# Performance work log

Hardware: AMD Instinct MI355X
Metric: run time of the kernel (lower is better)

Reference implementation:

```python
import jax, jax.numpy as jnp
import numpy as np

R = 2        # pixel-shuffle upscale
CN = 32      # channel_nums
COL = 3      # colors
NM = 6       # module_nums (2 convs each -> 12 backbone convs)
QMAX_A = 255.0   # uint8 activation fake-quant range
QMAX_W = 127.0   # int8 (narrow) weight fake-quant range


def fq_act(x, s):
    # Brevitas Uint8ActPerTensorFloat fake-quant with STE
    v = x / s
    q = jnp.clip(jnp.round(v), 0.0, QMAX_A)
    return s * (v + jax.lax.stop_gradient(q - v))


def fq_w(w, s):
    # Int8WeightPerTensorFloat (symmetric, narrow range) fake-quant with STE
    v = w / s
    q = jnp.clip(jnp.round(v), -QMAX_W, QMAX_W)
    return s * (v + jax.lax.stop_gradient(q - v))


def conv3(x, w, b):
    y = jax.lax.conv_general_dilated(
        x, w, window_strides=(1, 1), padding=((1, 1), (1, 1)),
        dimension_numbers=("NCHW", "OIHW", "NCHW"))
    return y + b[None, :, None, None]


def qblock(x, w, b, sw, act_s):
    # QuantConv3X3: quant_in -> quant conv (+bias) -> QuantReLU (relu + quant)
    xq = fq_act(x, act_s)
    y = conv3(xq, fq_w(w, sw), b)
    y = jax.nn.relu(y)
    return fq_act(y, act_s)


def pixel_shuffle(x, r):
    B, C, H, W = x.shape
    c = C // (r * r)
    x = x.reshape(B, c, r, r, H, W)
    x = x.transpose(0, 1, 4, 2, 5, 3)   # B, c, H, r, W, r
    return x.reshape(B, c, H * r, W * r)


def _forward(x, head_w, head_b, head_sw, bb_w, bb_b, bb_sw, tr_w, tr_b, tr_sw, act_s):
    y0 = qblock(x, head_w, head_b, head_sw, act_s)

    def step(y, p):
        w, b, sw = p
        return qblock(y, w, b, sw, act_s), None

    y, _ = jax.lax.scan(step, y0, (bb_w, bb_b, bb_sw))
    y = qblock(y + y0, tr_w, tr_b, tr_sw, act_s)   # act_type='linear' still hits QuantReLU branch
    y = jnp.clip(y, 0.0, 255.0)
    return pixel_shuffle(y, R)


def setup_inputs() -> dict:
    key = jax.random.key(0)
    ks = jax.random.split(key, 4)
    B, H, W = 8, 256, 256
    x = jax.random.uniform(ks[0], (B, COL, H, W), dtype=jnp.float32) * 255.0
    head_w = jax.random.normal(ks[1], (CN, COL, 3, 3), dtype=jnp.float32) * 0.05
    head_b = jnp.zeros((CN,), jnp.float32)
    bb_w = jax.random.normal(ks[2], (2 * NM, CN, CN, 3, 3), dtype=jnp.float32) * 0.05
    bb_b = jnp.zeros((2 * NM, CN), jnp.float32)
    tr_w = jax.random.normal(ks[3], (COL * R * R, CN, 3, 3), dtype=jnp.float32) * 0.05
    tr_b = jnp.zeros((COL * R * R,), jnp.float32)
    head_sw = jnp.max(jnp.abs(head_w)) / QMAX_W
    bb_sw = jnp.max(jnp.abs(bb_w), axis=(1, 2, 3, 4)) / QMAX_W
    tr_sw = jnp.max(jnp.abs(tr_w)) / QMAX_W
    act_s = jnp.float32(1.0)
    return dict(x=x, head_w=head_w, head_b=head_b, head_sw=head_sw,
                bb_w=bb_w, bb_b=bb_b, bb_sw=bb_sw,
                tr_w=tr_w, tr_b=tr_b, tr_sw=tr_sw, act_s=act_s)


def reference(x, head_w, head_b, head_sw, bb_w, bb_b, bb_sw, tr_w, tr_b, tr_sw, act_s):
    return _forward(x, head_w, head_b, head_sw, bb_w, bb_b, bb_sw, tr_w, tr_b, tr_sw, act_s)
```

## Files before the change

### kernel.cpp

```cpp
#include <hip/hip_runtime.h>

typedef int i32x4  __attribute__((ext_vector_type(4)));
typedef int i32x16 __attribute__((ext_vector_type(16)));

__global__ __launch_bounds__(256) void quantw_kernel(
    const float* __restrict__ src, float* __restrict__ dst,
    const float* __restrict__ sw, int per_layer_sw, int OC, int ICK, int total)
{
    int i = blockIdx.x * 256 + threadIdx.x;
    if (i >= total) return;
    int per = OC * ICK;
    int l = i / per;
    int rem = i - l * per;
    int oc = rem / ICK;
    int k = rem - oc * ICK;
    float s = sw[per_layer_sw ? l : 0];
    float v = rintf(src[i] / s);
    v = fminf(fmaxf(v, -127.0f), 127.0f);
    dst[l * per + k * OC + oc] = v;
}

__global__ __launch_bounds__(256) void packw_i8_kernel(
    const float* __restrict__ src, signed char* __restrict__ dst,
    const float* __restrict__ sw, int per_layer_sw, int OC_real, int total)
{
    int i = blockIdx.x * 256 + threadIdx.x;
    if (i >= total) return;
    int l   = i / 9216;
    int r   = i - l * 9216;
    int tap = r >> 10;
    int r2  = r & 1023;
    int lane = r2 >> 4;
    int j   = r2 & 15;
    int oc  = lane & 31;
    int ic  = ((lane >> 5) << 4) + j;
    signed char v = 0;
    if (oc < OC_real) {
        float s = sw[per_layer_sw ? l : 0];
        float q = rintf(src[((l * OC_real + oc) * 32 + ic) * 9 + tap] / s);
        q = fminf(fmaxf(q, -127.0f), 127.0f);
        v = (signed char)(int)q;
    }
    dst[i] = v;
}

__global__ __launch_bounds__(256) void wsum_kernel(
    const float* __restrict__ bb_w, const float* __restrict__ bb_sw,
    const float* __restrict__ tr_w, const float* __restrict__ tr_sw,
    float* __restrict__ wsum)
{
    int t = blockIdx.x * 256 + threadIdx.x;
    if (t >= 416) return;
    int l = t >> 5, oc = t & 31;
    float sum = 0.0f;
    if (l < 12) {
        float s = bb_sw[l];
        for (int k = 0; k < 288; ++k) {
            float q = rintf(bb_w[(l * 32 + oc) * 288 + k] / s);
            sum += fminf(fmaxf(q, -127.0f), 127.0f);
        }
    } else if (oc < 12) {
        float s = tr_sw[0];
        for (int k = 0; k < 288; ++k) {
            float q = rintf(tr_w[oc * 288 + k] / s);
            sum += fminf(fmaxf(q, -127.0f), 127.0f);
        }
    }
    wsum[t] = sum;
}

__global__ __launch_bounds__(256) void head_kernel(
    const float* __restrict__ x, const float* __restrict__ wq,
    const float* __restrict__ bias, const float* __restrict__ sw_ptr,
    const float* __restrict__ s_ptr, unsigned char* __restrict__ out)
{
    __shared__ unsigned char tile[3][10][34];
    const int tid = threadIdx.x;
    const int x0 = blockIdx.x * 32;
    const int y0 = blockIdx.y * 8;
    const int b  = blockIdx.z;
    const float s = s_ptr[0];

    for (int ch = 0; ch < 3; ++ch) {
        const int base = (b * 3 + ch) << 16;
        for (int p = tid; p < 10 * 34; p += 256) {
            int r = p / 34, c = p - r * 34;
            int gy = y0 + r - 1, gx = x0 + c - 1;
            unsigned char v = 0;
            if ((unsigned)gy < 256u && (unsigned)gx < 256u) {
                float xv = x[base + (gy << 8) + gx];
                float q = (s == 1.0f) ? xv : (xv / s);
                q = rintf(q);
                q = fminf(fmaxf(q, 0.0f), 255.0f);
                v = (unsigned char)q;
            }
            tile[ch][r][c] = v;
        }
    }
    __syncthreads();

    const int c = tid & 31, r = tid >> 5;
    float acc[32];
    #pragma unroll
    for (int i = 0; i < 32; ++i) acc[i] = 0.0f;

    #pragma unroll
    for (int ic = 0; ic < 3; ++ic) {
        float a[9];
        #pragma unroll
        for (int dy = 0; dy < 3; ++dy)
            #pragma unroll
            for (int dx = 0; dx < 3; ++dx)
                a[dy * 3 + dx] = (float)tile[ic][r + dy][c + dx];
        #pragma unroll
        for (int t = 0; t < 9; ++t) {
            const float* wrow = wq + (ic * 9 + t) * 32;
            #pragma unroll
            for (int oc = 0; oc < 32; ++oc)
                acc[oc] = fmaf(a[t], wrow[oc], acc[oc]);
        }
    }

    const float alpha = s * sw_ptr[0];
    unsigned int w8[8] = {0,0,0,0,0,0,0,0};
    #pragma unroll
    for (int oc = 0; oc < 32; ++oc) {
        float y = fmaf(alpha, acc[oc], bias[oc]);
        y = fmaxf(y, 0.0f);
        float v = (s == 1.0f) ? y : (y / s);
        v = rintf(v);
        v = fminf(fmaxf(v, 0.0f), 255.0f);
        w8[oc >> 2] |= ((unsigned int)(unsigned char)v) << (8 * (oc & 3));
    }
    uint4* dst = (uint4*)(out + (size_t)((((b << 8) + (y0 + r)) << 8) + (x0 + c)) * 32);
    dst[0] = make_uint4(w8[0] ^ 0x80808080u, w8[1] ^ 0x80808080u, w8[2] ^ 0x80808080u, w8[3] ^ 0x80808080u);
    dst[1] = make_uint4(w8[4] ^ 0x80808080u, w8[5] ^ 0x80808080u, w8[6] ^ 0x80808080u, w8[7] ^ 0x80808080u);
}

template<bool FINAL>
__global__ __launch_bounds__(256, 4) void qconv_i8_kernel(
    const unsigned char* __restrict__ in,
    const unsigned char* __restrict__ resid,
    const signed char* __restrict__ Wp,
    const float* __restrict__ bias,
    const float* __restrict__ wsum,
    const float* __restrict__ sw_ptr, int sw_idx,
    const float* __restrict__ s_ptr,
    void* __restrict__ out)
{
    __shared__ unsigned char aT[19584];
    const int tid = threadIdx.x;
    const int x0 = blockIdx.x << 5;
    const int y0 = blockIdx.y << 4;
    const int b  = blockIdx.z;

    #pragma unroll
    for (int it = 0; it < 5; ++it) {
        int ci = tid + it * 256;
        if (ci < 1224) {
            int row = (ci * 241) >> 14;
            int rem = ci - row * 68;
            int xt = rem >> 1, hf = rem & 1;
            int gy = y0 + row - 1, gx = x0 + xt - 1;
            uint4 v = make_uint4(0x80808080u, 0x80808080u, 0x80808080u, 0x80808080u);
            if ((unsigned)gy < 256u && (unsigned)gx < 256u) {
                size_t off = (size_t)((((b << 8) + gy) << 8) + gx) * 32 + (hf << 4);
                v = *(const uint4*)(in + off);
                if (FINAL) {
                    uint4 rv = *(const uint4*)(resid + off);
                    unsigned int* vp = (unsigned int*)&v;
                    const unsigned int* rp = (const unsigned int*)&rv;
                    #pragma unroll
                    for (int w = 0; w < 4; ++w) {
                        unsigned int xw = vp[w], yw = rp[w], ow = 0;
                        #pragma unroll
                        for (int bb = 0; bb < 4; ++bb) {
                            int xs = (int)(signed char)(xw >> (8 * bb));
                            int ys = (int)(signed char)(yw >> (8 * bb));
                            int t = xs + ys + 128;
                            if (t > 127) t = 127;
                            ow |= ((unsigned int)(t & 255)) << (8 * bb);
                        }
                        vp[w] = ow;
                    }
                }
            }
            int cs = rem ^ ((rem >> 3) & 7);
            *(uint4*)&aT[(row * 68 + cs) << 4] = v;
        }
    }
    __syncthreads();

    const int lane = tid & 63;
    const int wid  = tid >> 6;
    const int px   = lane & 31;
    const int khf  = lane >> 5;
    const int py0  = wid << 2;
    const int gx   = x0 + px;

    i32x16 acc[4];
    #pragma unroll
    for (int p = 0; p < 4; ++p)
        #pragma unroll
        for (int i = 0; i < 16; ++i) acc[p][i] = 0;

    #pragma unroll
    for (int dx = 0; dx < 3; ++dx) {
        const int c  = ((px + dx) << 1) + khf;
        const int cs = c ^ ((c >> 3) & 7);
        i32x4 af[6];
        #pragma unroll
        for (int yl = 0; yl < 6; ++yl)
            af[yl] = *(const i32x4*)&aT[((py0 + yl) * 68 + cs) << 4];
        #pragma unroll
        for (int dy = 0; dy < 3; ++dy) {
            i32x4 wf = *(const i32x4*)(Wp + ((((dy * 3 + dx) << 6) + lane) << 4));
            acc[0] = __builtin_amdgcn_mfma_i32_32x32x32_i8(wf, af[dy + 0], acc[0], 0, 0, 0);
            acc[1] = __builtin_amdgcn_mfma_i32_32x32x32_i8(wf, af[dy + 1], acc[1], 0, 0, 0);
            acc[2] = __builtin_amdgcn_mfma_i32_32x32x32_i8(wf, af[dy + 2], acc[2], 0, 0, 0);
            acc[3] = __builtin_amdgcn_mfma_i32_32x32x32_i8(wf, af[dy + 3], acc[3], 0, 0, 0);
        }
    }

    const float s = s_ptr[0];
    const float alpha = s * sw_ptr[sw_idx];

    if (!FINAL) {
        float bv[16];
        #pragma unroll
        for (int r = 0; r < 16; ++r) {
            const int oc = (r & 3) + ((r >> 2) << 3) + (khf << 2);
            bv[r] = fmaf(alpha * 128.0f, wsum[oc], bias[oc]);
        }
        #pragma unroll
        for (int py = 0; py < 4; ++py) {
            const int gy = y0 + py0 + py;
            unsigned char* pout = (unsigned char*)out + (((size_t)((((b << 8) + gy) << 8) + gx)) << 5);
            #pragma unroll
            for (int q = 0; q < 4; ++q) {
                unsigned int wv = 0;
                #pragma unroll
                for (int j = 0; j < 4; ++j) {
                    float y = fmaf(alpha, (float)acc[py][4 * q + j], bv[4 * q + j]);
                    y = fmaxf(y, 0.0f);
                    float v = (s == 1.0f) ? y : (y / s);
                    v = rintf(v);
                    v = fminf(fmaxf(v, 0.0f), 255.0f);
                    wv |= ((unsigned int)v) << (8 * j);
                }
                *(unsigned int*)(pout + 8 * q + 4 * khf) = wv ^ 0x80808080u;
            }
        }
    } else {
        #pragma unroll
        for (int py = 0; py < 4; ++py) {
            const int gy = y0 + py0 + py;
            #pragma unroll
            for (int r = 0; r < 16; ++r) {
                const int oc = (r & 3) + ((r >> 2) << 3) + (khf << 2);
                if (oc < 12) {
                    float y = fmaf(alpha, (float)acc[py][r],
                                   fmaf(alpha * 128.0f, wsum[oc], bias[oc]));
                    y = fmaxf(y, 0.0f);
                    float v = (s == 1.0f) ? y : (y / s);
                    v = rintf(v);
                    v = fminf(fmaxf(v, 0.0f), 255.0f);
                    float o = (s == 1.0f) ? v : fminf(fmaxf(s * v, 0.0f), 255.0f);
                    const int cc = oc >> 2, r1 = (oc >> 1) & 1, r2 = oc & 1;
                    ((float*)out)[(size_t)(((b * 3 + cc) << 9) + (gy << 1) + r1) * 512 + (gx << 1) + r2] = o;
                }
            }
        }
    }
}

extern "C" void kernel_launch(void* const* d_in, const int* in_sizes, int n_in,
                              void* d_out, int out_size, void* d_ws, size_t ws_size,
                              hipStream_t stream) {
    const float* x       = (const float*)d_in[0];
    const float* head_w  = (const float*)d_in[1];
    const float* head_b  = (const float*)d_in[2];
    const float* head_sw = (const float*)d_in[3];
    const float* bb_w    = (const float*)d_in[4];
    const float* bb_b    = (const float*)d_in[5];
    const float* bb_sw   = (const float*)d_in[6];
    const float* tr_w    = (const float*)d_in[7];
    const float* tr_b    = (const float*)d_in[8];
    const float* tr_sw   = (const float*)d_in[9];
    const float* act_s   = (const float*)d_in[10];

    char* ws = (char*)d_ws;
    unsigned char* buf0 = (unsigned char*)ws;
    unsigned char* buf1 = buf0 + 16777216;
    unsigned char* buf2 = buf1 + 16777216;
    float* wqH = (float*)(ws + 50331648);
    signed char* WpB = (signed char*)(ws + 50331648 + 4096);
    signed char* WpT = WpB + 110592;
    float* wsum = (float*)(ws + 50331648 + 4096 + 110592 + 9216);

    quantw_kernel<<<(864 + 255) / 256, 256, 0, stream>>>(head_w, wqH, head_sw, 0, 32, 27, 864);
    packw_i8_kernel<<<(110592 + 255) / 256, 256, 0, stream>>>(bb_w, WpB, bb_sw, 1, 32, 110592);
    packw_i8_kernel<<<(9216 + 255) / 256, 256, 0, stream>>>(tr_w, WpT, tr_sw, 0, 12, 9216);
    wsum_kernel<<<2, 256, 0, stream>>>(bb_w, bb_sw, tr_w, tr_sw, wsum);

    head_kernel<<<dim3(8, 32, 8), 256, 0, stream>>>(x, wqH, head_b, head_sw, act_s, buf0);

    dim3 gridB(8, 16, 8);
    const unsigned char* cur = buf0;
    unsigned char* nxt = buf1;
    for (int l = 0; l < 12; ++l) {
        qconv_i8_kernel<false><<<gridB, 256, 0, stream>>>(
            cur, nullptr, WpB + l * 9216, bb_b + l * 32, wsum + l * 32, bb_sw, l, act_s, (void*)nxt);
        cur = nxt;
        nxt = (nxt == buf1) ? buf2 : buf1;
    }

    qconv_i8_kernel<true><<<gridB, 256, 0, stream>>>(
        cur, buf0, WpT, tr_b, wsum + 384, tr_sw, 0, act_s, d_out);
}
```

Before: 355.9 us.

## Fuse consecutive backbone conv pairs into one kernel with halo recompute in LDS

Each pair of backbone 3x3 convs is now computed in a single 512-thread kernel. The first conv's output tile, including a one-pixel halo, is produced and kept in LDS as uint8, and the second conv reads it from there. This halves the number of global round-trips of the intermediate activations and the number of launches. In exchange it recomputes halo rows and columns (30-column output tiles computed from 32-column halo-expanded tiles), uses more LDS per block, and lowers occupancy.

```diff
diff --git a/kernel.cpp b/kernel.cpp
--- a/kernel.cpp
+++ b/kernel.cpp
@@ -137,16 +137,182 @@
     dst[1] = make_uint4(w8[4] ^ 0x80808080u, w8[5] ^ 0x80808080u, w8[6] ^ 0x80808080u, w8[7] ^ 0x80808080u);
 }
 
-template<bool FINAL>
-__global__ __launch_bounds__(256, 4) void qconv_i8_kernel(
+__global__ __launch_bounds__(512, 4) void qconv_pair_kernel(
+    const unsigned char* __restrict__ in,
+    const signed char* __restrict__ WpA, const signed char* __restrict__ WpB,
+    const float* __restrict__ biasA, const float* __restrict__ biasB,
+    const float* __restrict__ wsA, const float* __restrict__ wsB,
+    const float* __restrict__ sw_ptr, int idxA,
+    const float* __restrict__ s_ptr,
+    unsigned char* __restrict__ out)
+{
+    __shared__ uint4 lds[4624];
+    unsigned char* I8 = (unsigned char*)lds;
+    unsigned char* S8 = (unsigned char*)(lds + 2176);
+
+    const int tid = threadIdx.x;
+    const int x0 = blockIdx.x * 30;
+    const int y0 = blockIdx.y << 5;
+    const int b  = blockIdx.z;
+    const float s = s_ptr[0];
+
+    #pragma unroll
+    for (int it = 0; it < 5; ++it) {
+        int ci = tid + it * 512;
+        if (ci < 2448) {
+            int row = ci / 68, rem = ci - row * 68;
+            int xt = rem >> 1;
+            int gy = y0 + row - 2, gx = x0 + xt - 2;
+            uint4 v = make_uint4(0x80808080u, 0x80808080u, 0x80808080u, 0x80808080u);
+            if ((unsigned)gy < 256u && (unsigned)gx < 256u)
+                v = *(const uint4*)(in + (size_t)((((b << 8) + gy) << 8) + gx) * 32 + ((rem & 1) << 4));
+            int cs = rem ^ ((rem >> 3) & 7);
+            *(uint4*)&S8[(row * 68 + cs) << 4] = v;
+        }
+    }
+    __syncthreads();
+
+    const int lane = tid & 63;
+    const int wid  = tid >> 6;
+    const int px   = lane & 31;
+    const int khf  = lane >> 5;
+
+    {
+        const int ry0 = wid * 5;
+        i32x16 acc[5];
+        #pragma unroll
+        for (int p = 0; p < 5; ++p)
+            #pragma unroll
+            for (int i = 0; i < 16; ++i) acc[p][i] = 0;
+
+        #pragma unroll
+        for (int dx = 0; dx < 3; ++dx) {
+            int cc0 = ((px + dx) << 1) + khf;
+            int cs  = cc0 ^ ((cc0 >> 3) & 7);
+            i32x4 af[7];
+            #pragma unroll
+            for (int k = 0; k < 7; ++k) {
+                int jr = ry0 + k; if (jr > 35) jr = 35;
+                af[k] = *(const i32x4*)&S8[(jr * 68 + cs) << 4];
+            }
+            #pragma unroll
+            for (int dy = 0; dy < 3; ++dy) {
+                i32x4 wf = *(const i32x4*)(WpA + ((((dy * 3 + dx) << 6) + lane) << 4));
+                acc[0] = __builtin_amdgcn_mfma_i32_32x32x32_i8(wf, af[0 + dy], acc[0], 0, 0, 0);
+                acc[1] = __builtin_amdgcn_mfma_i32_32x32x32_i8(wf, af[1 + dy], acc[1], 0, 0, 0);
+                acc[2] = __builtin_amdgcn_mfma_i32_32x32x32_i8(wf, af[2 + dy], acc[2], 0, 0, 0);
+                acc[3] = __builtin_amdgcn_mfma_i32_32x32x32_i8(wf, af[3 + dy], acc[3], 0, 0, 0);
+                acc[4] = __builtin_amdgcn_mfma_i32_32x32x32_i8(wf, af[4 + dy], acc[4], 0, 0, 0);
+            }
+        }
+
+        const float alphaA = s * sw_ptr[idxA];
+        float bv[16];
+        #pragma unroll
+        for (int r = 0; r < 16; ++r) {
+            const int oc = (r & 3) + ((r >> 2) << 3) + (khf << 2);
+            bv[r] = fmaf(alphaA * 128.0f, wsA[oc], biasA[oc]);
+        }
+        const int gxi = x0 - 1 + px;
+        const bool colOK = (unsigned)gxi < 256u;
+        #pragma unroll
+        for (int a = 0; a < 5; ++a) {
+            const int j = ry0 + a;
+            if (j < 34) {
+                const int gyi = y0 - 1 + j;
+                const bool ok = colOK && ((unsigned)gyi < 256u);
+                #pragma unroll
+                for (int q = 0; q < 4; ++q) {
+                    unsigned int wv = 0;
+                    if (ok) {
+                        #pragma unroll
+                        for (int j2 = 0; j2 < 4; ++j2) {
+                            float y = fmaf(alphaA, (float)acc[a][4 * q + j2], bv[4 * q + j2]);
+                            y = fmaxf(y, 0.0f);
+                            float v = (s == 1.0f) ? y : (y / s);
+                            v = rintf(v);
+                            v = fminf(fmaxf(v, 0.0f), 255.0f);
+                            wv |= ((unsigned int)v) << (8 * j2);
+                        }
+                    }
+                    int h = q >> 1;
+                    int cc0 = (px << 1) + h;
+                    int cs = cc0 ^ ((cc0 >> 3) & 7);
+                    *(unsigned int*)&I8[((j * 64 + cs) << 4) + ((q & 1) << 3) + (khf << 2)] = wv ^ 0x80808080u;
+                }
+            }
+        }
+    }
+    __syncthreads();
+
+    {
+        const int py0 = wid << 2;
+        i32x16 acc[4];
+        #pragma unroll
+        for (int p = 0; p < 4; ++p)
+            #pragma unroll
+            for (int i = 0; i < 16; ++i) acc[p][i] = 0;
+
+        #pragma unroll
+        for (int dx = 0; dx < 3; ++dx) {
+            int c = px + dx; if (c > 31) c = 31;
+            int cc0 = (c << 1) + khf;
+            int cs  = cc0 ^ ((cc0 >> 3) & 7);
+            i32x4 af[6];
+            #pragma unroll
+            for (int k = 0; k < 6; ++k)
+                af[k] = *(const i32x4*)&I8[((py0 + k) * 64 + cs) << 4];
+            #pragma unroll
+            for (int dy = 0; dy < 3; ++dy) {
+                i32x4 wf = *(const i32x4*)(WpB + ((((dy * 3 + dx) << 6) + lane) << 4));
+                acc[0] = __builtin_amdgcn_mfma_i32_32x32x32_i8(wf, af[0 + dy], acc[0], 0, 0, 0);
+                acc[1] = __builtin_amdgcn_mfma_i32_32x32x32_i8(wf, af[1 + dy], acc[1], 0, 0, 0);
+                acc[2] = __builtin_amdgcn_mfma_i32_32x32x32_i8(wf, af[2 + dy], acc[2], 0, 0, 0);
+                acc[3] = __builtin_amdgcn_mfma_i32_32x32x32_i8(wf, af[3 + dy], acc[3], 0, 0, 0);
+            }
+        }
+
+        const float alphaB = s * sw_ptr[idxA + 1];
+        float bv[16];
+        #pragma unroll
+        for (int r = 0; r < 16; ++r) {
+            const int oc = (r & 3) + ((r >> 2) << 3) + (khf << 2);
+            bv[r] = fmaf(alphaB * 128.0f, wsB[oc], biasB[oc]);
+        }
+        const int gxo = x0 + px;
+        if (px < 30 && gxo < 256) {
+            #pragma unroll
+            for (int py = 0; py < 4; ++py) {
+                const int gy = y0 + py0 + py;
+                unsigned char* pout = out + (((size_t)((((b << 8) + gy) << 8) + gxo)) << 5);
+                #pragma unroll
+                for (int q = 0; q < 4; ++q) {
+                    unsigned int wv = 0;
+                    #pragma unroll
+                    for (int j2 = 0; j2 < 4; ++j2) {
+                        float y = fmaf(alphaB, (float)acc[py][4 * q + j2], bv[4 * q + j2]);
+                        y = fmaxf(y, 0.0f);
+                        float v = (s == 1.0f) ? y : (y / s);
+                        v = rintf(v);
+                        v = fminf(fmaxf(v, 0.0f), 255.0f);
+                        wv |= ((unsigned int)v) << (8 * j2);
+                    }
+                    *(unsigned int*)(pout + 8 * q + 4 * khf) = wv ^ 0x80808080u;
+                }
+            }
+        }
+    }
+}
+
+__global__ __launch_bounds__(256, 4) void qconv_tail_kernel(
     const unsigned char* __restrict__ in,
     const unsigned char* __restrict__ resid,
     const signed char* __restrict__ Wp,
     const float* __restrict__ bias,
     const float* __restrict__ wsum,
-    const float* __restrict__ sw_ptr, int sw_idx,
+    const float* __restrict__ sw_ptr,
     const float* __restrict__ s_ptr,
-    void* __restrict__ out)
+    float* __restrict__ out)
 {
     __shared__ unsigned char aT[19584];
     const int tid = threadIdx.x;
@@ -158,7 +324,7 @@
     for (int it = 0; it < 5; ++it) {
         int ci = tid + it * 256;
         if (ci < 1224) {
-            int row = (ci * 241) >> 14;
+            int row = ci / 68;
             int rem = ci - row * 68;
             int xt = rem >> 1, hf = rem & 1;
             int gy = y0 + row - 1, gx = x0 + xt - 1;
@@ -166,23 +332,21 @@
             if ((unsigned)gy < 256u && (unsigned)gx < 256u) {
                 size_t off = (size_t)((((b << 8) + gy) << 8) + gx) * 32 + (hf << 4);
                 v = *(const uint4*)(in + off);
-                if (FINAL) {
-                    uint4 rv = *(const uint4*)(resid + off);
-                    unsigned int* vp = (unsigned int*)&v;
-                    const unsigned int* rp = (const unsigned int*)&rv;
+                uint4 rv = *(const uint4*)(resid + off);
+                unsigned int* vp = (unsigned int*)&v;
+                const unsigned int* rp = (const unsigned int*)&rv;
+                #pragma unroll
+                for (int w = 0; w < 4; ++w) {
+                    unsigned int xw = vp[w], yw = rp[w], ow = 0;
                     #pragma unroll
-                    for (int w = 0; w < 4; ++w) {
-                        unsigned int xw = vp[w], yw = rp[w], ow = 0;
-                        #pragma unroll
-                        for (int bb = 0; bb < 4; ++bb) {
-                            int xs = (int)(signed char)(xw >> (8 * bb));
-                            int ys = (int)(signed char)(yw >> (8 * bb));
-                            int t = xs + ys + 128;
-                            if (t > 127) t = 127;
-                            ow |= ((unsigned int)(t & 255)) << (8 * bb);
-                        }
-                        vp[w] = ow;
+                    for (int bb = 0; bb < 4; ++bb) {
+                        int xs = (int)(signed char)(xw >> (8 * bb));
+                        int ys = (int)(signed char)(yw >> (8 * bb));
+                        int t = xs + ys + 128;
+                        if (t > 127) t = 127;
+                        ow |= ((unsigned int)(t & 255)) << (8 * bb);
                     }
+                    vp[w] = ow;
                 }
             }
             int cs = rem ^ ((rem >> 3) & 7);
@@ -215,60 +379,31 @@
         #pragma unroll
         for (int dy = 0; dy < 3; ++dy) {
             i32x4 wf = *(const i32x4*)(Wp + ((((dy * 3 + dx) << 6) + lane) << 4));
-            acc[0] = __builtin_amdgcn_mfma_i32_32x32x32_i8(wf, af[dy + 0], acc[0], 0, 0, 0);
-            acc[1] = __builtin_amdgcn_mfma_i32_32x32x32_i8(wf, af[dy + 1], acc[1], 0, 0, 0);
-            acc[2] = __builtin_amdgcn_mfma_i32_32x32x32_i8(wf, af[dy + 2], acc[2], 0, 0, 0);
-            acc[3] = __builtin_amdgcn_mfma_i32_32x32x32_i8(wf, af[dy + 3], acc[3], 0, 0, 0);
+            acc[0] = __builtin_amdgcn_mfma_i32_32x32x32_i8(wf, af[0 + dy], acc[0], 0, 0, 0);
+            acc[1] = __builtin_amdgcn_mfma_i32_32x32x32_i8(wf, af[1 + dy], acc[1], 0, 0, 0);
+            acc[2] = __builtin_amdgcn_mfma_i32_32x32x32_i8(wf, af[2 + dy], acc[2], 0, 0, 0);
+            acc[3] = __builtin_amdgcn_mfma_i32_32x32x32_i8(wf, af[3 + dy], acc[3], 0, 0, 0);
         }
     }
 
     const float s = s_ptr[0];
-    const float alpha = s * sw_ptr[sw_idx];
-
-    if (!FINAL) {
-        float bv[16];
+    const float alpha = s * sw_ptr[0];
+    #pragma unroll
+    for (int py = 0; py < 4; ++py) {
+        const int gy = y0 + py0 + py;
         #pragma unroll
         for (int r = 0; r < 16; ++r) {
             const int oc = (r & 3) + ((r >> 2) << 3) + (khf << 2);
-            bv[r] = fmaf(alpha * 128.0f, wsum[oc], bias[oc]);
-        }
-        #pragma unroll
-        for (int py = 0; py < 4; ++py) {
-            const int gy = y0 + py0 + py;
-            unsigned char* pout = (unsigned char*)out + (((size_t)((((b << 8) + gy) << 8) + gx)) << 5);
-            #pragma unroll
-            for (int q = 0; q < 4; ++q) {
-                unsigned int wv = 0;
-                #pragma unroll
-                for (int j = 0; j < 4; ++j) {
-                    float y = fmaf(alpha, (float)acc[py][4 * q + j], bv[4 * q + j]);
-                    y = fmaxf(y, 0.0f);
-                    float v = (s == 1.0f) ? y : (y / s);
-                    v = rintf(v);
-                    v = fminf(fmaxf(v, 0.0f), 255.0f);
-                    wv |= ((unsigned int)v) << (8 * j);
-                }
-                *(unsigned int*)(pout + 8 * q + 4 * khf) = wv ^ 0x80808080u;
-            }
-        }
-    } else {
-        #pragma unroll
-        for (int py = 0; py < 4; ++py) {
-            const int gy = y0 + py0 + py;
-            #pragma unroll
-            for (int r = 0; r < 16; ++r) {
-                const int oc = (r & 3) + ((r >> 2) << 3) + (khf << 2);
-                if (oc < 12) {
-                    float y = fmaf(alpha, (float)acc[py][r],
-                                   fmaf(alpha * 128.0f, wsum[oc], bias[oc]));
-                    y = fmaxf(y, 0.0f);
-                    float v = (s == 1.0f) ? y : (y / s);
-                    v = rintf(v);
-                    v = fminf(fmaxf(v, 0.0f), 255.0f);
-                    float o = (s == 1.0f) ? v : fminf(fmaxf(s * v, 0.0f), 255.0f);
-                    const int cc = oc >> 2, r1 = (oc >> 1) & 1, r2 = oc & 1;
-                    ((float*)out)[(size_t)(((b * 3 + cc) << 9) + (gy << 1) + r1) * 512 + (gx << 1) + r2] = o;
-                }
+            if (oc < 12) {
+                float y = fmaf(alpha, (float)acc[py][r],
+                               fmaf(alpha * 128.0f, wsum[oc], bias[oc]));
+                y = fmaxf(y, 0.0f);
+                float v = (s == 1.0f) ? y : (y / s);
+                v = rintf(v);
+                v = fminf(fmaxf(v, 0.0f), 255.0f);
+                float o = (s == 1.0f) ? v : fminf(fmaxf(s * v, 0.0f), 255.0f);
+                const int cc = oc >> 2, r1 = (oc >> 1) & 1, r2 = oc & 1;
+                out[(size_t)(((b * 3 + cc) << 9) + (gy << 1) + r1) * 512 + (gx << 1) + r2] = o;
             }
         }
     }
@@ -305,16 +440,20 @@
 
     head_kernel<<<dim3(8, 32, 8), 256, 0, stream>>>(x, wqH, head_b, head_sw, act_s, buf0);
 
-    dim3 gridB(8, 16, 8);
+    dim3 gridP(9, 8, 8);
     const unsigned char* cur = buf0;
     unsigned char* nxt = buf1;
-    for (int l = 0; l < 12; ++l) {
-        qconv_i8_kernel<false><<<gridB, 256, 0, stream>>>(
-            cur, nullptr, WpB + l * 9216, bb_b + l * 32, wsum + l * 32, bb_sw, l, act_s, (void*)nxt);
+    for (int p = 0; p < 6; ++p) {
+        qconv_pair_kernel<<<gridP, 512, 0, stream>>>(
+            cur,
+            WpB + (2 * p) * 9216, WpB + (2 * p + 1) * 9216,
+            bb_b + (2 * p) * 32, bb_b + (2 * p + 1) * 32,
+            wsum + (2 * p) * 32, wsum + (2 * p + 1) * 32,
+            bb_sw, 2 * p, act_s, nxt);
         cur = nxt;
         nxt = (nxt == buf1) ? buf2 : buf1;
     }
 
-    qconv_i8_kernel<true><<<gridB, 256, 0, stream>>>(
-        cur, buf0, WpT, tr_b, wsum + 384, tr_sw, 0, act_s, d_out);
-}
+    qconv_tail_kernel<<<dim3(8, 16, 8), 256, 0, stream>>>(
+        cur, buf0, WpT, tr_b, wsum + 384, tr_sw, act_s, (float*)d_out);
+}
```

Measured after the change: 390.6 us. 1.1x slower.
